# Performance work log

Hardware: AMD Instinct MI355X
Metric: run time of the kernel (lower is better)

The kernel has to match this reference:

```python
import jax, jax.numpy as jnp
import numpy as np

BETA = 0.25  # commitment loss weight (init kwarg)


def setup_inputs() -> dict:
    key = jax.random.key(0)
    k1, k2 = jax.random.split(key)
    z = jax.random.normal(k1, (16, 32, 32, 256), dtype=jnp.float32)
    embedding = jax.random.normal(k2, (8192, 256), dtype=jnp.float32)
    return {"z": z, "embedding": embedding}


def reference(z, embedding):
    # Eval-mode forward of EMAVectorQuantizer (EMA buffer update only runs in training).
    b, h, w, c = z.shape
    zf = z.reshape(-1, c)  # [N, d]
    # Squared L2 distance to every codebook entry: ||z||^2 + ||e||^2 - 2 z.e
    d = (jnp.sum(zf * zf, axis=1, keepdims=True)
         + jnp.sum(embedding * embedding, axis=1)
         - 2.0 * jnp.einsum('nd,kd->nk', zf, embedding))  # [N, n_embed]
    idx = jnp.argmin(d, axis=1)  # [N]
    z_q = embedding[idx].reshape(z.shape)  # codebook gather

    # Commitment loss (z_q is detached in the original)
    diff = BETA * jnp.mean((jax.lax.stop_gradient(z_q) - z) ** 2)

    # Straight-through estimator
    z_q = z + jax.lax.stop_gradient(z_q - z)
    z_q = jnp.transpose(z_q, (0, 3, 1, 2))  # b h w c -> b c h w

    # Perplexity as written in the source: each one-hot row contributes
    # exactly 1*log(1 + 1e-12), so the mean is a constant == exp(-log1p(1e-12)).
    perplexity = jnp.exp(-jnp.log1p(jnp.float32(1e-12)))

    return z_q, diff, idx, perplexity
```

## Files before the change

kernel.cpp:

```cpp
#include <hip/hip_runtime.h>
#include <hip/hip_bf16.h>
#include <hip/hip_fp16.h>

#define N_VEC   16384
#define K_CODES 8192
#define D_DIM   256
#define NSPLIT  8
#define KT_PER  8
#define BM      128

#define ZQ_SIZE  (16*256*32*32)
#define DIFF_OFF ZQ_SIZE
#define IDX_OFF  (ZQ_SIZE + 1)
#define PERP_OFF (ZQ_SIZE + 1 + N_VEC)

#define WS_ENORM 0
#define WS_ZH    65536
#define WS_EH    (WS_ZH + N_VEC * D_DIM * 2)
#define WS_P2    (WS_EH + K_CODES * D_DIM * 2)
#define WS_IDXI  (WS_P2 + NSPLIT * N_VEC * 16)
#define WS_LOSS  (WS_IDXI + N_VEC * 4)

typedef _Float16 f16x8 __attribute__((ext_vector_type(8)));
typedef float    f32x4 __attribute__((ext_vector_type(4)));

__device__ __forceinline__ unsigned long long skey(float s, int c) {
    unsigned u = __float_as_uint(s);
    u ^= (unsigned)((int)u >> 31) | 0x80000000u;
    return ((unsigned long long)u << 13) | (unsigned)c;
}

__device__ __forceinline__ int swz_off(int row, int dloc) {
    return row * 128 + ((((dloc >> 3) ^ (row & 7))) << 4) + ((dloc & 7) << 1);
}

__device__ __forceinline__ void gload16(const void* g, void* l) {
    __builtin_amdgcn_global_load_lds((const __attribute__((address_space(1))) unsigned int*)g,
                                     (__attribute__((address_space(3))) unsigned int*)l,
                                     16, 0, 0);
}

__global__ __launch_bounds__(256) void convert_kernel(const float* __restrict__ Z,
                                                      const float* __restrict__ E,
                                                      char* __restrict__ ws) {
    const int t  = threadIdx.x;
    const int r  = blockIdx.x * 4 + (t >> 6);
    const int d0 = (t & 63) * 4;
    const float* src;
    char* dh;
    const bool isE = (r >= N_VEC);
    if (!isE) {
        src = Z + (size_t)r * D_DIM;
        const int rowl = r & 127;
        dh = ws + WS_ZH + (size_t)(((r >> 7) * 4) + (d0 >> 6)) * 16384
           + swz_off(rowl, d0 & 63);
    } else {
        const int re = r - N_VEC;
        src = E + (size_t)re * D_DIM;
        const int col  = re & 127;
        const int k32  = d0 >> 5;
        const int dloc = d0 & 31;
        const int slot = (dloc >> 3) ^ ((col >> 1) & 3);
        dh = ws + WS_EH + (size_t)((re >> 7) * 8 + k32) * 8192
           + col * 64 + slot * 16 + (dloc & 7) * 2;
    }
    const float4 v = *reinterpret_cast<const float4*>(src + d0);
    const unsigned h0 = __half_as_ushort(__float2half(v.x));
    const unsigned h1 = __half_as_ushort(__float2half(v.y));
    const unsigned h2 = __half_as_ushort(__float2half(v.z));
    const unsigned h3 = __half_as_ushort(__float2half(v.w));
    uint2 hi;
    hi.x = h0 | (h1 << 16);  hi.y = h2 | (h3 << 16);
    *reinterpret_cast<uint2*>(dh) = hi;

    if (isE) {
        float s = v.x * v.x + v.y * v.y + v.z * v.z + v.w * v.w;
        #pragma unroll
        for (int off = 32; off; off >>= 1) s += __shfl_down(s, off);
        if ((t & 63) == 0) ((float*)(ws + WS_ENORM))[r - N_VEC] = s;
    }
}

__global__ __launch_bounds__(256, 2) void vq_mfma_kernel(const char* __restrict__ ws_ro,
                                                         ulonglong2* __restrict__ part2) {
    __shared__ short lds[40960];

    const int tid  = threadIdx.x;
    const int lane = tid & 63, wid = tid >> 6;
    const int lane15 = lane & 15, g = lane >> 4;
    const int l7  = lane15 & 7;
    const int c13 = (lane15 >> 1) & 3;
    const int wm = wid >> 1, wn = wid & 1;
    const int bx = blockIdx.x, ksp = blockIdx.y;
    const int row0 = bx * BM;
    const int kbase = ksp * (K_CODES / NSPLIT);

    const char* zh = ws_ro + WS_ZH;
    const char* eh = ws_ro + WS_EH;
    const float* enorm = (const float*)(ws_ro + WS_ENORM);

    #define STAGE_B(kt_, j_)                                                           \
    do {                                                                               \
        const char* sB = eh + (size_t)(((ksp * 8 + (kt_)) * 8) + (j_)) * 8192          \
                            + wid * 2048 + lane * 16;                                  \
        short* dB = lds + 32768 + ((j_) & 1) * 4096 + wid * 1024 + lane * 8;           \
        gload16(sB, dB);                                                               \
        gload16(sB + 1024, dB + 512);                                                  \
    } while (0)

    {
        const char* srcA = zh + (size_t)bx * 65536 + wid * 16384 + lane * 16;
        short* dA = lds + wid * 8192 + lane * 8;
        #pragma unroll
        for (int i = 0; i < 16; ++i) gload16(srcA + i * 1024, dA + i * 512);
    }
    STAGE_B(0, 0);
    float en_c[4], en_n[4];
    #pragma unroll
    for (int n = 0; n < 4; ++n) en_c[n] = enorm[kbase + wn * 64 + n * 16 + lane15];
    asm volatile("s_waitcnt vmcnt(0)" ::: "memory");
    __builtin_amdgcn_s_barrier();
    __builtin_amdgcn_sched_barrier(0);

    int rowterm[4];
    #pragma unroll
    for (int m = 0; m < 4; ++m) rowterm[m] = (wm * 64 + m * 16 + lane15) * 64;
    int colterm[4];
    #pragma unroll
    for (int n = 0; n < 4; ++n) colterm[n] = (wn * 64 + n * 16 + lane15) * 32;
    const int sa0 = (g ^ l7) * 8;
    const int sb  = (g ^ c13) * 8;

    float bestv[16];
    int   bestc[16];
    #pragma unroll
    for (int i = 0; i < 16; ++i) { bestv[i] = 3.0e38f; bestc[i] = 0; }

    #define STEP(j_)                                                                   \
    do {                                                                               \
        asm volatile("s_waitcnt vmcnt(0)" ::: "memory");                               \
        __builtin_amdgcn_s_barrier();                                                  \
        __builtin_amdgcn_sched_barrier(0);                                             \
        f16x8 af[4], bf[4];                                                            \
        const int abase = ((j_) >> 1) * 8192 + (sa0 ^ (((j_) & 1) << 5));              \
        const int bbase = 32768 + ((j_) & 1) * 4096 + sb;                              \
        _Pragma("unroll")                                                              \
        for (int m = 0; m < 4; ++m)                                                    \
            af[m] = *reinterpret_cast<const f16x8*>(lds + abase + rowterm[m]);         \
        _Pragma("unroll")                                                              \
        for (int n = 0; n < 4; ++n)                                                    \
            bf[n] = *reinterpret_cast<const f16x8*>(lds + bbase + colterm[n]);         \
        if ((j_) < 7) {                                                                \
            STAGE_B(kt, (j_) + 1);                                                     \
        } else if (kt < KT_PER - 1) {                                                  \
            STAGE_B(kt + 1, 0);                                                        \
            _Pragma("unroll")                                                          \
            for (int n = 0; n < 4; ++n)                                                \
                en_n[n] = enorm[kbase + (kt + 1) * 128 + wn * 64 + n * 16 + lane15];   \
        }                                                                              \
        __builtin_amdgcn_s_setprio(1);                                                 \
        _Pragma("unroll")                                                              \
        for (int m = 0; m < 4; ++m)                                                    \
            _Pragma("unroll")                                                          \
            for (int n = 0; n < 4; ++n)                                                \
                acc[m][n] = __builtin_amdgcn_mfma_f32_16x16x32_f16(                    \
                    af[m], bf[n], acc[m][n], 0, 0, 0);                                 \
        __builtin_amdgcn_s_setprio(0);                                                 \
    } while (0)

    for (int kt = 0; kt < KT_PER; ++kt) {
        f32x4 acc[4][4];
        #pragma unroll
        for (int m = 0; m < 4; ++m)
            #pragma unroll
            for (int n = 0; n < 4; ++n)
                #pragma unroll
                for (int q = 0; q < 4; ++q) acc[m][n][q] = 0.0f;

        STEP(0); STEP(1); STEP(2); STEP(3);
        STEP(4); STEP(5); STEP(6); STEP(7);

        #pragma unroll
        for (int m = 0; m < 4; ++m)
            #pragma unroll
            for (int n = 0; n < 4; ++n) {
                const int c = kbase + kt * 128 + wn * 64 + n * 16 + lane15;
                #pragma unroll
                for (int q = 0; q < 4; ++q) {
                    const int sl = m * 4 + q;
                    const float s = fmaf(-2.0f, acc[m][n][q], en_c[n]);
                    if (s < bestv[sl]) { bestv[sl] = s; bestc[sl] = c; }
                }
            }
        #pragma unroll
        for (int n = 0; n < 4; ++n) en_c[n] = en_n[n];
    }
    #undef STEP
    #undef STAGE_B

    unsigned long long* t2 = reinterpret_cast<unsigned long long*>(lds);
    #pragma unroll
    for (int sl = 0; sl < 16; ++sl) {
        const int m = sl >> 2, q = sl & 3;
        const unsigned long long k1 = skey(bestv[sl], bestc[sl]);
        unsigned long long m1 = k1;
        #pragma unroll
        for (int msk = 1; msk < 16; msk <<= 1) {
            const unsigned long long o = __shfl_xor(m1, msk);
            m1 = (o < m1) ? o : m1;
        }
        unsigned long long k2 = (k1 == m1) ? ~0ull : k1;
        #pragma unroll
        for (int msk = 1; msk < 16; msk <<= 1) {
            const unsigned long long o = __shfl_xor(k2, msk);
            k2 = (o < k2) ? o : k2;
        }
        if (lane15 == 0) {
            const int row64 = m * 16 + g * 4 + q;
            t2[(wid * 64 + row64) * 2 + 0] = m1;
            t2[(wid * 64 + row64) * 2 + 1] = k2;
        }
    }
    __syncthreads();
    if (tid < 128) {
        const int wm2 = tid >> 6, r64 = tid & 63;
        const unsigned long long a1 = t2[((wm2 * 2 + 0) * 64 + r64) * 2 + 0];
        const unsigned long long a2 = t2[((wm2 * 2 + 0) * 64 + r64) * 2 + 1];
        const unsigned long long b1 = t2[((wm2 * 2 + 1) * 64 + r64) * 2 + 0];
        const unsigned long long b2 = t2[((wm2 * 2 + 1) * 64 + r64) * 2 + 1];
        const unsigned long long r1 = (a1 < b1) ? a1 : b1;
        const unsigned long long hi = (a1 < b1) ? b1 : a1;
        const unsigned long long l2 = (a2 < b2) ? a2 : b2;
        const unsigned long long r2 = (hi < l2) ? hi : l2;
        ulonglong2 res;  res.x = r1;  res.y = r2;
        part2[(size_t)ksp * N_VEC + row0 + tid] = res;
    }
}

__global__ __launch_bounds__(256) void rescore_kernel(const float* __restrict__ Z,
                                                      const float* __restrict__ E,
                                                      const ulonglong2* __restrict__ part2,
                                                      int* __restrict__ idx_i,
                                                      float* __restrict__ out_idx,
                                                      float* __restrict__ lossp) {
    __shared__ double redl[4];
    const int tid = threadIdx.x, lane = tid & 63, wid = tid >> 6;
    const int r = blockIdx.x * 4 + wid;
    int c0 = 0, c1 = 0, c2 = 0, c3 = 0;
    if (lane == 0) {
        unsigned long long m0 = ~0ull, m1 = ~0ull, m2 = ~0ull, m3 = ~0ull;
        for (int s = 0; s < NSPLIT; ++s) {
            const ulonglong2 p = part2[(size_t)s * N_VEC + r];
            unsigned long long k = p.x;
            if (k < m0) { m3 = m2; m2 = m1; m1 = m0; m0 = k; }
            else if (k < m1) { m3 = m2; m2 = m1; m1 = k; }
            else if (k < m2) { m3 = m2; m2 = k; }
            else if (k < m3) { m3 = k; }
            k = p.y;
            if (k < m0) { m3 = m2; m2 = m1; m1 = m0; m0 = k; }
            else if (k < m1) { m3 = m2; m2 = m1; m1 = k; }
            else if (k < m2) { m3 = m2; m2 = k; }
            else if (k < m3) { m3 = k; }
        }
        c0 = (int)(m0 & 0x1FFFull);  c1 = (int)(m1 & 0x1FFFull);
        c2 = (int)(m2 & 0x1FFFull);  c3 = (int)(m3 & 0x1FFFull);
    }
    c0 = __shfl(c0, 0);  c1 = __shfl(c1, 0);
    c2 = __shfl(c2, 0);  c3 = __shfl(c3, 0);
    const float4 z4 = *reinterpret_cast<const float4*>(Z + (size_t)r * D_DIM + lane * 4);
    double d[4];
    const int cc[4] = {c0, c1, c2, c3};
    #pragma unroll
    for (int j = 0; j < 4; ++j) {
        const float4 e4 = *reinterpret_cast<const float4*>(E + (size_t)cc[j] * D_DIM + lane * 4);
        const double ax = (double)z4.x - (double)e4.x, ay = (double)z4.y - (double)e4.y;
        const double az = (double)z4.z - (double)e4.z, aw = (double)z4.w - (double)e4.w;
        d[j] = ax * ax + ay * ay + az * az + aw * aw;
    }
    #pragma unroll
    for (int off = 1; off < 64; off <<= 1) {
        #pragma unroll
        for (int j = 0; j < 4; ++j) d[j] += __shfl_xor(d[j], off);
    }
    if (lane == 0) {
        double bd = d[0];  int bi = c0;
        #pragma unroll
        for (int j = 1; j < 4; ++j) {
            if (d[j] < bd || (d[j] == bd && cc[j] < bi)) { bd = d[j]; bi = cc[j]; }
        }
        idx_i[r]   = bi;
        out_idx[r] = (float)bi;
        redl[wid]  = bd;
    }
    __syncthreads();
    if (tid == 0) lossp[blockIdx.x] = (float)(redl[0] + redl[1] + redl[2] + redl[3]);
}

__global__ __launch_bounds__(256) void gather_kernel(const float* __restrict__ E,
                                                     const int* __restrict__ idx_i,
                                                     float* __restrict__ out) {
    __shared__ float Ls[128 * 65];
    __shared__ int   sIdx[64];

    const int tid = threadIdx.x;
    const int gb  = blockIdx.x;
    const int n0  = gb * 64;
    const int b   = n0 >> 10;
    const int hwbase = n0 & 1023;

    if (tid < 64) sIdx[tid] = idx_i[n0 + tid];
    __syncthreads();

    for (int h = 0; h < 2; ++h) {
        if (h) __syncthreads();
        const int rowl = tid >> 2;
        const int qs   = tid & 3;
        const float* erow = E + (size_t)sIdx[rowl] * D_DIM + h * 128;
        #pragma unroll
        for (int m = 0; m < 8; ++m) {
            const int c4 = m * 4 + qs;
            const float4 v = *reinterpret_cast<const float4*>(erow + c4 * 4);
            Ls[(c4 * 4 + 0) * 65 + rowl] = v.x;
            Ls[(c4 * 4 + 1) * 65 + rowl] = v.y;
            Ls[(c4 * 4 + 2) * 65 + rowl] = v.z;
            Ls[(c4 * 4 + 3) * 65 + rowl] = v.w;
        }
        __syncthreads();
        const int wl   = tid & 63;
        const int csub = tid >> 6;
        #pragma unroll
        for (int pc = 0; pc < 32; ++pc) {
            const int c_l = pc * 4 + csub;
            const int c   = h * 128 + c_l;
            out[((size_t)(b * 256 + c)) * 1024 + hwbase + wl] = Ls[c_l * 65 + wl];
        }
    }
}

__global__ __launch_bounds__(256) void final_kernel(const float* __restrict__ lossp,
                                                    float* __restrict__ out) {
    __shared__ float red[4];
    const int tid = threadIdx.x;
    float s = 0.0f;
    for (int i = tid; i < N_VEC / 4; i += 256) s += lossp[i];
    #pragma unroll
    for (int off = 32; off; off >>= 1) s += __shfl_down(s, off);
    if ((tid & 63) == 0) red[tid >> 6] = s;
    __syncthreads();
    if (tid == 0) {
        const float total = red[0] + red[1] + red[2] + red[3];
        out[DIFF_OFF] = 0.25f * (total / (float)(N_VEC * D_DIM));
        out[PERP_OFF] = 1.0f;
    }
}

extern "C" void kernel_launch(void* const* d_in, const int* in_sizes, int n_in,
                              void* d_out, int out_size, void* d_ws, size_t ws_size,
                              hipStream_t stream) {
    const float* Z = (const float*)d_in[0];
    const float* E = (const float*)d_in[1];
    float* out = (float*)d_out;
    char*  ws  = (char*)d_ws;

    ulonglong2* part2   = (ulonglong2*)(ws + WS_P2);
    int*        idx_i   = (int*)(ws + WS_IDXI);
    float*      lossbuf = (float*)(ws + WS_LOSS);

    hipLaunchKernelGGL(convert_kernel, dim3((N_VEC + K_CODES) / 4), dim3(256), 0, stream, Z, E, ws);
    hipLaunchKernelGGL(vq_mfma_kernel, dim3(N_VEC / BM, NSPLIT), dim3(256), 0, stream,
                       (const char*)ws, part2);
    hipLaunchKernelGGL(rescore_kernel, dim3(N_VEC / 4), dim3(256), 0, stream,
                       Z, E, part2, idx_i, out + IDX_OFF, lossbuf);
    hipLaunchKernelGGL(gather_kernel, dim3(N_VEC / 64), dim3(256), 0, stream,
                       E, idx_i, out);
    hipLaunchKernelGGL(final_kernel, dim3(1), dim3(256), 0, stream, lossbuf, out);
}
```

Measured before the change: 117.5 us.

## Hold A tile in registers and stream codebook through a 4-slot LDS ring

```diff
diff --git a/kernel.cpp b/kernel.cpp
--- a/kernel.cpp
+++ b/kernel.cpp
@@ -39,6 +39,9 @@
                                      (__attribute__((address_space(3))) unsigned int*)l,
                                      16, 0, 0);
 }
+
+#define VMW__(n) asm volatile("s_waitcnt vmcnt(" #n ")" ::: "memory")
+#define VMW(n) VMW__(n)
 
 __global__ __launch_bounds__(256) void convert_kernel(const float* __restrict__ Z,
                                                       const float* __restrict__ E,
@@ -83,124 +86,127 @@
 
 __global__ __launch_bounds__(256, 2) void vq_mfma_kernel(const char* __restrict__ ws_ro,
                                                          ulonglong2* __restrict__ part2) {
-    __shared__ short lds[40960];
+    __shared__ short lds[18432];
 
     const int tid  = threadIdx.x;
     const int lane = tid & 63, wid = tid >> 6;
     const int lane15 = lane & 15, g = lane >> 4;
-    const int l7  = lane15 & 7;
     const int c13 = (lane15 >> 1) & 3;
-    const int wm = wid >> 1, wn = wid & 1;
     const int bx = blockIdx.x, ksp = blockIdx.y;
     const int row0 = bx * BM;
     const int kbase = ksp * (K_CODES / NSPLIT);
+    const int kspBase = ksp * 64;
 
     const char* zh = ws_ro + WS_ZH;
     const char* eh = ws_ro + WS_EH;
-    const float* enorm = (const float*)(ws_ro + WS_ENORM);
-
-    #define STAGE_B(kt_, j_)                                                           \
+    short* ring = lds;
+    float* enl  = (float*)(lds + 16384);
+
+    #define STAGE_SC(sc_, slot_)                                                       \
     do {                                                                               \
-        const char* sB = eh + (size_t)(((ksp * 8 + (kt_)) * 8) + (j_)) * 8192          \
-                            + wid * 2048 + lane * 16;                                  \
-        short* dB = lds + 32768 + ((j_) & 1) * 4096 + wid * 1024 + lane * 8;           \
+        const char* sB = eh + (size_t)(kspBase + (sc_)) * 8192 + wid * 2048 + lane * 16; \
+        short* dB = ring + (slot_) * 4096 + wid * 1024 + lane * 8;                     \
         gload16(sB, dB);                                                               \
         gload16(sB + 1024, dB + 512);                                                  \
     } while (0)
 
+    f16x8 areg[8][2];
     {
-        const char* srcA = zh + (size_t)bx * 65536 + wid * 16384 + lane * 16;
-        short* dA = lds + wid * 8192 + lane * 8;
-        #pragma unroll
-        for (int i = 0; i < 16; ++i) gload16(srcA + i * 1024, dA + i * 512);
-    }
-    STAGE_B(0, 0);
-    float en_c[4], en_n[4];
-    #pragma unroll
-    for (int n = 0; n < 4; ++n) en_c[n] = enorm[kbase + wn * 64 + n * 16 + lane15];
-    asm volatile("s_waitcnt vmcnt(0)" ::: "memory");
+        const char* tileA = zh + (size_t)bx * 65536;
+        #pragma unroll
+        for (int j = 0; j < 8; ++j)
+            #pragma unroll
+            for (int m = 0; m < 2; ++m) {
+                const int row  = wid * 32 + m * 16 + lane15;
+                const int slot = (((j & 1) * 4 + g)) ^ (row & 7);
+                areg[j][m] = *reinterpret_cast<const f16x8*>(
+                    tileA + (j >> 1) * 16384 + row * 128 + (slot << 4));
+            }
+    }
+    gload16((const char*)(ws_ro + WS_ENORM) + ksp * 4096 + wid * 1024 + lane * 16,
+            (char*)enl + wid * 1024 + lane * 16);
+    __builtin_amdgcn_sched_barrier(0);
+    STAGE_SC(0, 0);
+    STAGE_SC(1, 1);
+    STAGE_SC(2, 2);
+    #pragma unroll
+    for (int j = 0; j < 8; ++j)
+        #pragma unroll
+        for (int m = 0; m < 2; ++m)
+            asm volatile("" : "+v"(areg[j][m]));
+
+    int colterm[8];
+    #pragma unroll
+    for (int n = 0; n < 8; ++n) colterm[n] = (n * 16 + lane15) * 32;
+    const int sb = (g ^ c13) * 8;
+
+    float bestv[8];
+    int   bestc[8];
+    #pragma unroll
+    for (int i = 0; i < 8; ++i) { bestv[i] = 3.0e38f; bestc[i] = 0; }
+
+    VMW(6);
     __builtin_amdgcn_s_barrier();
     __builtin_amdgcn_sched_barrier(0);
 
-    int rowterm[4];
-    #pragma unroll
-    for (int m = 0; m < 4; ++m) rowterm[m] = (wm * 64 + m * 16 + lane15) * 64;
-    int colterm[4];
-    #pragma unroll
-    for (int n = 0; n < 4; ++n) colterm[n] = (wn * 64 + n * 16 + lane15) * 32;
-    const int sa0 = (g ^ l7) * 8;
-    const int sb  = (g ^ c13) * 8;
-
-    float bestv[16];
-    int   bestc[16];
-    #pragma unroll
-    for (int i = 0; i < 16; ++i) { bestv[i] = 3.0e38f; bestc[i] = 0; }
-
-    #define STEP(j_)                                                                   \
+    #define STEP(j_, c_)                                                               \
     do {                                                                               \
-        asm volatile("s_waitcnt vmcnt(0)" ::: "memory");                               \
+        VMW(c_);                                                                       \
         __builtin_amdgcn_s_barrier();                                                  \
         __builtin_amdgcn_sched_barrier(0);                                             \
-        f16x8 af[4], bf[4];                                                            \
-        const int abase = ((j_) >> 1) * 8192 + (sa0 ^ (((j_) & 1) << 5));              \
-        const int bbase = 32768 + ((j_) & 1) * 4096 + sb;                              \
+        f16x8 bf[8];                                                                   \
         _Pragma("unroll")                                                              \
-        for (int m = 0; m < 4; ++m)                                                    \
-            af[m] = *reinterpret_cast<const f16x8*>(lds + abase + rowterm[m]);         \
-        _Pragma("unroll")                                                              \
-        for (int n = 0; n < 4; ++n)                                                    \
-            bf[n] = *reinterpret_cast<const f16x8*>(lds + bbase + colterm[n]);         \
-        if ((j_) < 7) {                                                                \
-            STAGE_B(kt, (j_) + 1);                                                     \
-        } else if (kt < KT_PER - 1) {                                                  \
-            STAGE_B(kt + 1, 0);                                                        \
-            _Pragma("unroll")                                                          \
-            for (int n = 0; n < 4; ++n)                                                \
-                en_n[n] = enorm[kbase + (kt + 1) * 128 + wn * 64 + n * 16 + lane15];   \
-        }                                                                              \
+        for (int n_ = 0; n_ < 8; ++n_)                                                 \
+            bf[n_] = *reinterpret_cast<const f16x8*>(ring + ((j_) & 3) * 4096          \
+                                                     + colterm[n_] + sb);              \
+        const int sc_ = kt * 8 + (j_) + 3;                                             \
+        if (sc_ < 64) STAGE_SC(sc_, ((j_) + 3) & 3);                                   \
         __builtin_amdgcn_s_setprio(1);                                                 \
         _Pragma("unroll")                                                              \
-        for (int m = 0; m < 4; ++m)                                                    \
+        for (int m_ = 0; m_ < 2; ++m_)                                                 \
             _Pragma("unroll")                                                          \
-            for (int n = 0; n < 4; ++n)                                                \
-                acc[m][n] = __builtin_amdgcn_mfma_f32_16x16x32_f16(                    \
-                    af[m], bf[n], acc[m][n], 0, 0, 0);                                 \
+            for (int n_ = 0; n_ < 8; ++n_)                                             \
+                acc[m_][n_] = __builtin_amdgcn_mfma_f32_16x16x32_f16(                  \
+                    areg[j_][m_], bf[n_], acc[m_][n_], 0, 0, 0);                       \
         __builtin_amdgcn_s_setprio(0);                                                 \
     } while (0)
 
     for (int kt = 0; kt < KT_PER; ++kt) {
-        f32x4 acc[4][4];
-        #pragma unroll
-        for (int m = 0; m < 4; ++m)
+        float en_r[8];
+        #pragma unroll
+        for (int n = 0; n < 8; ++n) en_r[n] = enl[kt * 128 + n * 16 + lane15];
+
+        f32x4 acc[2][8];
+        #pragma unroll
+        for (int m = 0; m < 2; ++m)
             #pragma unroll
-            for (int n = 0; n < 4; ++n)
+            for (int n = 0; n < 8; ++n)
                 #pragma unroll
                 for (int q = 0; q < 4; ++q) acc[m][n][q] = 0.0f;
 
-        STEP(0); STEP(1); STEP(2); STEP(3);
-        STEP(4); STEP(5); STEP(6); STEP(7);
-
-        #pragma unroll
-        for (int m = 0; m < 4; ++m)
+        STEP(0, 4); STEP(1, 4); STEP(2, 4);
+        STEP(3, 4); STEP(4, 4); STEP(5, 4);
+        if (kt < KT_PER - 1) { STEP(6, 4); STEP(7, 4); }
+        else                 { STEP(6, 2); STEP(7, 0); }
+
+        #pragma unroll
+        for (int m = 0; m < 2; ++m)
             #pragma unroll
-            for (int n = 0; n < 4; ++n) {
-                const int c = kbase + kt * 128 + wn * 64 + n * 16 + lane15;
+            for (int n = 0; n < 8; ++n) {
+                const int c = kbase + kt * 128 + n * 16 + lane15;
                 #pragma unroll
                 for (int q = 0; q < 4; ++q) {
                     const int sl = m * 4 + q;
-                    const float s = fmaf(-2.0f, acc[m][n][q], en_c[n]);
+                    const float s = fmaf(-2.0f, acc[m][n][q], en_r[n]);
                     if (s < bestv[sl]) { bestv[sl] = s; bestc[sl] = c; }
                 }
             }
-        #pragma unroll
-        for (int n = 0; n < 4; ++n) en_c[n] = en_n[n];
     }
     #undef STEP
-    #undef STAGE_B
-
-    unsigned long long* t2 = reinterpret_cast<unsigned long long*>(lds);
-    #pragma unroll
-    for (int sl = 0; sl < 16; ++sl) {
+    #undef STAGE_SC
+
+    #pragma unroll
+    for (int sl = 0; sl < 8; ++sl) {
         const int m = sl >> 2, q = sl & 3;
         const unsigned long long k1 = skey(bestv[sl], bestc[sl]);
         unsigned long long m1 = k1;
@@ -216,24 +222,10 @@
             k2 = (o < k2) ? o : k2;
         }
         if (lane15 == 0) {
-            const int row64 = m * 16 + g * 4 + q;
-            t2[(wid * 64 + row64) * 2 + 0] = m1;
-            t2[(wid * 64 + row64) * 2 + 1] = k2;
-        }
-    }
-    __syncthreads();
-    if (tid < 128) {
-        const int wm2 = tid >> 6, r64 = tid & 63;
-        const unsigned long long a1 = t2[((wm2 * 2 + 0) * 64 + r64) * 2 + 0];
-        const unsigned long long a2 = t2[((wm2 * 2 + 0) * 64 + r64) * 2 + 1];
-        const unsigned long long b1 = t2[((wm2 * 2 + 1) * 64 + r64) * 2 + 0];
-        const unsigned long long b2 = t2[((wm2 * 2 + 1) * 64 + r64) * 2 + 1];
-        const unsigned long long r1 = (a1 < b1) ? a1 : b1;
-        const unsigned long long hi = (a1 < b1) ? b1 : a1;
-        const unsigned long long l2 = (a2 < b2) ? a2 : b2;
-        const unsigned long long r2 = (hi < l2) ? hi : l2;
-        ulonglong2 res;  res.x = r1;  res.y = r2;
-        part2[(size_t)ksp * N_VEC + row0 + tid] = res;
+            const int row = row0 + wid * 32 + m * 16 + g * 4 + q;
+            ulonglong2 res;  res.x = m1;  res.y = k2;
+            part2[(size_t)ksp * N_VEC + row] = res;
+        }
     }
 }
 
```

Result: slower. 152.8 us (+30.1%).

## Widen VQ MFMA block to 512 threads with 256-code tiles and triple-buffered ring

Applied to the files above, without the earlier changes.

```diff
diff --git a/kernel.cpp b/kernel.cpp
--- a/kernel.cpp
+++ b/kernel.cpp
@@ -6,7 +6,6 @@
 #define K_CODES 8192
 #define D_DIM   256
 #define NSPLIT  8
-#define KT_PER  8
 #define BM      128
 
 #define ZQ_SIZE  (16*256*32*32)
@@ -39,6 +38,9 @@
                                      (__attribute__((address_space(3))) unsigned int*)l,
                                      16, 0, 0);
 }
+
+#define VMW__(n) asm volatile("s_waitcnt vmcnt(" #n ")" ::: "memory")
+#define VMW(n) VMW__(n)
 
 __global__ __launch_bounds__(256) void convert_kernel(const float* __restrict__ Z,
                                                       const float* __restrict__ E,
@@ -81,94 +83,97 @@
     }
 }
 
-__global__ __launch_bounds__(256, 2) void vq_mfma_kernel(const char* __restrict__ ws_ro,
+__global__ __launch_bounds__(512, 2) void vq_mfma_kernel(const char* __restrict__ ws_ro,
                                                          ulonglong2* __restrict__ part2) {
-    __shared__ short lds[40960];
+    __shared__ short lds[59392];
 
     const int tid  = threadIdx.x;
     const int lane = tid & 63, wid = tid >> 6;
     const int lane15 = lane & 15, g = lane >> 4;
     const int l7  = lane15 & 7;
-    const int c13 = (lane15 >> 1) & 3;
-    const int wm = wid >> 1, wn = wid & 1;
+    const int wm = wid >> 2, wn = wid & 3;
     const int bx = blockIdx.x, ksp = blockIdx.y;
     const int row0 = bx * BM;
     const int kbase = ksp * (K_CODES / NSPLIT);
 
     const char* zh = ws_ro + WS_ZH;
     const char* eh = ws_ro + WS_EH;
-    const float* enorm = (const float*)(ws_ro + WS_ENORM);
-
-    #define STAGE_B(kt_, j_)                                                           \
+    short* ring = lds + 32768;
+    float* enl  = (float*)(lds + 57344);
+
+    #define STAGE_SC(sc_, slot_)                                                       \
     do {                                                                               \
-        const char* sB = eh + (size_t)(((ksp * 8 + (kt_)) * 8) + (j_)) * 8192          \
-                            + wid * 2048 + lane * 16;                                  \
-        short* dB = lds + 32768 + ((j_) & 1) * 4096 + wid * 1024 + lane * 8;           \
-        gload16(sB, dB);                                                               \
-        gload16(sB + 1024, dB + 512);                                                  \
+        if ((sc_) < 32) {                                                              \
+            const int cg_ = (sc_) >> 3, j_ = (sc_) & 7;                                \
+            const char* s0 = eh + (size_t)(((ksp * 8 + cg_ * 2) * 8) + j_) * 8192      \
+                                + wid * 1024 + lane * 16;                              \
+            short* d_ = ring + (slot_) * 8192 + wid * 512 + lane * 8;                  \
+            gload16(s0, d_);                                                           \
+            gload16(s0 + 65536, d_ + 4096);                                            \
+        }                                                                              \
     } while (0)
 
     {
-        const char* srcA = zh + (size_t)bx * 65536 + wid * 16384 + lane * 16;
-        short* dA = lds + wid * 8192 + lane * 8;
-        #pragma unroll
-        for (int i = 0; i < 16; ++i) gload16(srcA + i * 1024, dA + i * 512);
-    }
-    STAGE_B(0, 0);
-    float en_c[4], en_n[4];
-    #pragma unroll
-    for (int n = 0; n < 4; ++n) en_c[n] = enorm[kbase + wn * 64 + n * 16 + lane15];
-    asm volatile("s_waitcnt vmcnt(0)" ::: "memory");
+        const char* srcA = zh + (size_t)bx * 65536 + wid * 8192 + lane * 16;
+        short* dA = lds + wid * 4096 + lane * 8;
+        #pragma unroll
+        for (int i = 0; i < 8; ++i) gload16(srcA + i * 1024, dA + i * 512);
+    }
+    gload16((const char*)(ws_ro + WS_ENORM) + ksp * 4096 + (wid & 3) * 1024 + lane * 16,
+            (char*)enl + (wid & 3) * 1024 + lane * 16);
+    __builtin_amdgcn_sched_barrier(0);
+    STAGE_SC(0, 0);
+    STAGE_SC(1, 1);
+
+    int rowterm[4];
+    #pragma unroll
+    for (int m = 0; m < 4; ++m) rowterm[m] = (wm * 64 + m * 16 + lane15) * 64;
+    const int sa0 = (g ^ l7) * 8;
+    int boff[4];
+    #pragma unroll
+    for (int n = 0; n < 4; ++n) {
+        const int cl   = wn * 64 + n * 16 + lane15;
+        const int c127 = cl & 127;
+        boff[n] = (cl >> 7) * 4096 + c127 * 32 + ((g ^ ((c127 >> 1) & 3)) << 3);
+    }
+
+    float bestv[16];
+    int   bestc[16];
+    #pragma unroll
+    for (int i = 0; i < 16; ++i) { bestv[i] = 3.0e38f; bestc[i] = 0; }
+
+    VMW(2);
     __builtin_amdgcn_s_barrier();
     __builtin_amdgcn_sched_barrier(0);
 
-    int rowterm[4];
-    #pragma unroll
-    for (int m = 0; m < 4; ++m) rowterm[m] = (wm * 64 + m * 16 + lane15) * 64;
-    int colterm[4];
-    #pragma unroll
-    for (int n = 0; n < 4; ++n) colterm[n] = (wn * 64 + n * 16 + lane15) * 32;
-    const int sa0 = (g ^ l7) * 8;
-    const int sb  = (g ^ c13) * 8;
-
-    float bestv[16];
-    int   bestc[16];
-    #pragma unroll
-    for (int i = 0; i < 16; ++i) { bestv[i] = 3.0e38f; bestc[i] = 0; }
-
-    #define STEP(j_)                                                                   \
+    #define STEP(cg_, j_)                                                              \
     do {                                                                               \
-        asm volatile("s_waitcnt vmcnt(0)" ::: "memory");                               \
+        const int s_ = (cg_) * 8 + (j_);                                               \
+        if (s_ == 31) { VMW(0); } else { VMW(2); }                                     \
         __builtin_amdgcn_s_barrier();                                                  \
         __builtin_amdgcn_sched_barrier(0);                                             \
         f16x8 af[4], bf[4];                                                            \
         const int abase = ((j_) >> 1) * 8192 + (sa0 ^ (((j_) & 1) << 5));              \
-        const int bbase = 32768 + ((j_) & 1) * 4096 + sb;                              \
+        const int bbase = (s_ % 3) * 8192;                                             \
         _Pragma("unroll")                                                              \
-        for (int m = 0; m < 4; ++m)                                                    \
-            af[m] = *reinterpret_cast<const f16x8*>(lds + abase + rowterm[m]);         \
+        for (int m_ = 0; m_ < 4; ++m_)                                                 \
+            af[m_] = *reinterpret_cast<const f16x8*>(lds + abase + rowterm[m_]);       \
         _Pragma("unroll")                                                              \
-        for (int n = 0; n < 4; ++n)                                                    \
-            bf[n] = *reinterpret_cast<const f16x8*>(lds + bbase + colterm[n]);         \
-        if ((j_) < 7) {                                                                \
-            STAGE_B(kt, (j_) + 1);                                                     \
-        } else if (kt < KT_PER - 1) {                                                  \
-            STAGE_B(kt + 1, 0);                                                        \
-            _Pragma("unroll")                                                          \
-            for (int n = 0; n < 4; ++n)                                                \
-                en_n[n] = enorm[kbase + (kt + 1) * 128 + wn * 64 + n * 16 + lane15];   \
-        }                                                                              \
+        for (int n_ = 0; n_ < 4; ++n_)                                                 \
+            bf[n_] = *reinterpret_cast<const f16x8*>(ring + bbase + boff[n_]);         \
+        STAGE_SC(s_ + 2, (s_ + 2) % 3);                                                \
         __builtin_amdgcn_s_setprio(1);                                                 \
         _Pragma("unroll")                                                              \
-        for (int m = 0; m < 4; ++m)                                                    \
+        for (int m_ = 0; m_ < 4; ++m_)                                                 \
             _Pragma("unroll")                                                          \
-            for (int n = 0; n < 4; ++n)                                                \
-                acc[m][n] = __builtin_amdgcn_mfma_f32_16x16x32_f16(                    \
-                    af[m], bf[n], acc[m][n], 0, 0, 0);                                 \
+            for (int n_ = 0; n_ < 4; ++n_)                                             \
+                acc[m_][n_] = __builtin_amdgcn_mfma_f32_16x16x32_f16(                  \
+                    af[m_], bf[n_], acc[m_][n_], 0, 0, 0);                             \
         __builtin_amdgcn_s_setprio(0);                                                 \
     } while (0)
 
-    for (int kt = 0; kt < KT_PER; ++kt) {
+    #pragma unroll
+    for (int cg = 0; cg < 4; ++cg) {
         f32x4 acc[4][4];
         #pragma unroll
         for (int m = 0; m < 4; ++m)
@@ -177,27 +182,28 @@
                 #pragma unroll
                 for (int q = 0; q < 4; ++q) acc[m][n][q] = 0.0f;
 
-        STEP(0); STEP(1); STEP(2); STEP(3);
-        STEP(4); STEP(5); STEP(6); STEP(7);
+        STEP(cg, 0); STEP(cg, 1); STEP(cg, 2); STEP(cg, 3);
+        STEP(cg, 4); STEP(cg, 5); STEP(cg, 6); STEP(cg, 7);
 
         #pragma unroll
         for (int m = 0; m < 4; ++m)
             #pragma unroll
             for (int n = 0; n < 4; ++n) {
-                const int c = kbase + kt * 128 + wn * 64 + n * 16 + lane15;
+                const int cl = cg * 256 + wn * 64 + n * 16 + lane15;
+                const int c  = kbase + cl;
+                const float en = enl[cl];
                 #pragma unroll
                 for (int q = 0; q < 4; ++q) {
                     const int sl = m * 4 + q;
-                    const float s = fmaf(-2.0f, acc[m][n][q], en_c[n]);
+                    const float s = fmaf(-2.0f, acc[m][n][q], en);
                     if (s < bestv[sl]) { bestv[sl] = s; bestc[sl] = c; }
                 }
             }
-        #pragma unroll
-        for (int n = 0; n < 4; ++n) en_c[n] = en_n[n];
     }
     #undef STEP
-    #undef STAGE_B
-
+    #undef STAGE_SC
+
+    __syncthreads();
     unsigned long long* t2 = reinterpret_cast<unsigned long long*>(lds);
     #pragma unroll
     for (int sl = 0; sl < 16; ++sl) {
@@ -223,17 +229,19 @@
     }
     __syncthreads();
     if (tid < 128) {
-        const int wm2 = tid >> 6, r64 = tid & 63;
-        const unsigned long long a1 = t2[((wm2 * 2 + 0) * 64 + r64) * 2 + 0];
-        const unsigned long long a2 = t2[((wm2 * 2 + 0) * 64 + r64) * 2 + 1];
-        const unsigned long long b1 = t2[((wm2 * 2 + 1) * 64 + r64) * 2 + 0];
-        const unsigned long long b2 = t2[((wm2 * 2 + 1) * 64 + r64) * 2 + 1];
-        const unsigned long long r1 = (a1 < b1) ? a1 : b1;
-        const unsigned long long hi = (a1 < b1) ? b1 : a1;
-        const unsigned long long l2 = (a2 < b2) ? a2 : b2;
-        const unsigned long long r2 = (hi < l2) ? hi : l2;
-        ulonglong2 res;  res.x = r1;  res.y = r2;
-        part2[(size_t)ksp * N_VEC + row0 + tid] = res;
+        const int wmg = tid >> 6, r64 = tid & 63;
+        unsigned long long m0 = ~0ull, m1 = ~0ull;
+        #pragma unroll
+        for (int w = 0; w < 4; ++w) {
+            #pragma unroll
+            for (int k = 0; k < 2; ++k) {
+                const unsigned long long key = t2[(((wmg * 4 + w) * 64) + r64) * 2 + k];
+                if (key < m0) { m1 = m0; m0 = key; }
+                else if (key < m1) { m1 = key; }
+            }
+        }
+        ulonglong2 res;  res.x = m0;  res.y = m1;
+        part2[(size_t)ksp * N_VEC + row0 + wmg * 64 + r64] = res;
     }
 }
 
@@ -367,7 +375,7 @@
     float*      lossbuf = (float*)(ws + WS_LOSS);
 
     hipLaunchKernelGGL(convert_kernel, dim3((N_VEC + K_CODES) / 4), dim3(256), 0, stream, Z, E, ws);
-    hipLaunchKernelGGL(vq_mfma_kernel, dim3(N_VEC / BM, NSPLIT), dim3(256), 0, stream,
+    hipLaunchKernelGGL(vq_mfma_kernel, dim3(N_VEC / BM, NSPLIT), dim3(512), 0, stream,
                        (const char*)ws, part2);
     hipLaunchKernelGGL(rescore_kernel, dim3(N_VEC / 4), dim3(256), 0, stream,
                        Z, E, part2, idx_i, out + IDX_OFF, lossbuf);
```

Result: slower. 147.3 us (+25.4%).

## Switch to 16x16x16 MFMA with a 4-slot codebook ring and partial waits

Applied to the files above, without the earlier changes.

```diff
diff --git a/kernel.cpp b/kernel.cpp
--- a/kernel.cpp
+++ b/kernel.cpp
@@ -21,7 +21,7 @@
 #define WS_IDXI  (WS_P2 + NSPLIT * N_VEC * 16)
 #define WS_LOSS  (WS_IDXI + N_VEC * 4)
 
-typedef _Float16 f16x8 __attribute__((ext_vector_type(8)));
+typedef _Float16 f16x4 __attribute__((ext_vector_type(4)));
 typedef float    f32x4 __attribute__((ext_vector_type(4)));
 
 __device__ __forceinline__ unsigned long long skey(float s, int c) {
@@ -39,6 +39,9 @@
                                      (__attribute__((address_space(3))) unsigned int*)l,
                                      16, 0, 0);
 }
+
+#define VMW__(n) asm volatile("s_waitcnt vmcnt(" #n ")" ::: "memory")
+#define VMW(n) VMW__(n)
 
 __global__ __launch_bounds__(256) void convert_kernel(const float* __restrict__ Z,
                                                       const float* __restrict__ E,
@@ -57,12 +60,10 @@
     } else {
         const int re = r - N_VEC;
         src = E + (size_t)re * D_DIM;
-        const int col  = re & 127;
-        const int k32  = d0 >> 5;
-        const int dloc = d0 & 31;
-        const int slot = (dloc >> 3) ^ ((col >> 1) & 3);
-        dh = ws + WS_EH + (size_t)((re >> 7) * 8 + k32) * 8192
-           + col * 64 + slot * 16 + (dloc & 7) * 2;
+        const int col = re & 127;
+        const int q   = (d0 >> 2) & 3;
+        dh = ws + WS_EH + (size_t)((re >> 7) * 16 + (d0 >> 4)) * 4096
+           + col * 32 + ((q ^ ((col >> 2) & 3)) << 3);
     }
     const float4 v = *reinterpret_cast<const float4*>(src + d0);
     const unsigned h0 = __half_as_ushort(__float2half(v.x));
@@ -88,8 +89,7 @@
     const int tid  = threadIdx.x;
     const int lane = tid & 63, wid = tid >> 6;
     const int lane15 = lane & 15, g = lane >> 4;
-    const int l7  = lane15 & 7;
-    const int c13 = (lane15 >> 1) & 3;
+    const int g1 = g >> 1;
     const int wm = wid >> 1, wn = wid & 1;
     const int bx = blockIdx.x, ksp = blockIdx.y;
     const int row0 = bx * BM;
@@ -98,14 +98,13 @@
     const char* zh = ws_ro + WS_ZH;
     const char* eh = ws_ro + WS_EH;
     const float* enorm = (const float*)(ws_ro + WS_ENORM);
-
-    #define STAGE_B(kt_, j_)                                                           \
+    short* ring = lds + 32768;
+
+    #define STAGE_C(kt_, pp_)                                                          \
     do {                                                                               \
-        const char* sB = eh + (size_t)(((ksp * 8 + (kt_)) * 8) + (j_)) * 8192          \
-                            + wid * 2048 + lane * 16;                                  \
-        short* dB = lds + 32768 + ((j_) & 1) * 4096 + wid * 1024 + lane * 8;           \
-        gload16(sB, dB);                                                               \
-        gload16(sB + 1024, dB + 512);                                                  \
+        const char* sC = eh + (size_t)(((ksp * 8 + (kt_)) * 16) + (pp_)) * 4096        \
+                            + tid * 16;                                                \
+        gload16(sC, ring + ((pp_) & 3) * 2048 + tid * 8);                              \
     } while (0)
 
     {
@@ -114,57 +113,56 @@
         #pragma unroll
         for (int i = 0; i < 16; ++i) gload16(srcA + i * 1024, dA + i * 512);
     }
-    STAGE_B(0, 0);
-    float en_c[4], en_n[4];
-    #pragma unroll
-    for (int n = 0; n < 4; ++n) en_c[n] = enorm[kbase + wn * 64 + n * 16 + lane15];
-    asm volatile("s_waitcnt vmcnt(0)" ::: "memory");
+    STAGE_C(0, 0);
+    STAGE_C(0, 1);
+    VMW(1);
     __builtin_amdgcn_s_barrier();
     __builtin_amdgcn_sched_barrier(0);
 
-    int rowterm[4];
-    #pragma unroll
-    for (int m = 0; m < 4; ++m) rowterm[m] = (wm * 64 + m * 16 + lane15) * 64;
-    int colterm[4];
-    #pragma unroll
-    for (int n = 0; n < 4; ++n) colterm[n] = (wn * 64 + n * 16 + lane15) * 32;
-    const int sa0 = (g ^ l7) * 8;
-    const int sb  = (g ^ c13) * 8;
+    int rowbase[4], r7[4];
+    #pragma unroll
+    for (int m = 0; m < 4; ++m) {
+        const int row = wm * 64 + m * 16 + lane15;
+        rowbase[m] = row * 64 + 4 * (g & 1);
+        r7[m]      = row & 7;
+    }
+    int boffn[4];
+    #pragma unroll
+    for (int n = 0; n < 4; ++n) {
+        const int col = wn * 64 + n * 16 + lane15;
+        boffn[n] = col * 16 + ((g ^ ((col >> 2) & 3)) << 2);
+    }
 
     float bestv[16];
     int   bestc[16];
     #pragma unroll
     for (int i = 0; i < 16; ++i) { bestv[i] = 3.0e38f; bestc[i] = 0; }
 
-    #define STEP(j_)                                                                   \
+    #define STEP(p_)                                                                   \
     do {                                                                               \
-        asm volatile("s_waitcnt vmcnt(0)" ::: "memory");                               \
+        if ((p_) == 15 && kt == KT_PER - 1) { VMW(0); } else { VMW(1); }               \
         __builtin_amdgcn_s_barrier();                                                  \
         __builtin_amdgcn_sched_barrier(0);                                             \
-        f16x8 af[4], bf[4];                                                            \
-        const int abase = ((j_) >> 1) * 8192 + (sa0 ^ (((j_) & 1) << 5));              \
-        const int bbase = 32768 + ((j_) & 1) * 4096 + sb;                              \
+        f16x4 af[4], bf[4];                                                            \
+        const int abase = ((p_) >> 2) * 8192;                                          \
+        const int op    = ((p_) & 3) * 2;                                              \
         _Pragma("unroll")                                                              \
-        for (int m = 0; m < 4; ++m)                                                    \
-            af[m] = *reinterpret_cast<const f16x8*>(lds + abase + rowterm[m]);         \
+        for (int m_ = 0; m_ < 4; ++m_)                                                 \
+            af[m_] = *reinterpret_cast<const f16x4*>(                                  \
+                lds + abase + rowbase[m_] + (((op + g1) ^ r7[m_]) << 3));              \
         _Pragma("unroll")                                                              \
-        for (int n = 0; n < 4; ++n)                                                    \
-            bf[n] = *reinterpret_cast<const f16x8*>(lds + bbase + colterm[n]);         \
-        if ((j_) < 7) {                                                                \
-            STAGE_B(kt, (j_) + 1);                                                     \
-        } else if (kt < KT_PER - 1) {                                                  \
-            STAGE_B(kt + 1, 0);                                                        \
-            _Pragma("unroll")                                                          \
-            for (int n = 0; n < 4; ++n)                                                \
-                en_n[n] = enorm[kbase + (kt + 1) * 128 + wn * 64 + n * 16 + lane15];   \
-        }                                                                              \
+        for (int n_ = 0; n_ < 4; ++n_)                                                 \
+            bf[n_] = *reinterpret_cast<const f16x4*>(                                  \
+                ring + ((p_) & 3) * 2048 + boffn[n_]);                                 \
+        if ((p_) < 14)                STAGE_C(kt, (p_) + 2);                           \
+        else if (kt < KT_PER - 1)     STAGE_C(kt + 1, (p_) - 14);                      \
         __builtin_amdgcn_s_setprio(1);                                                 \
         _Pragma("unroll")                                                              \
-        for (int m = 0; m < 4; ++m)                                                    \
+        for (int m_ = 0; m_ < 4; ++m_)                                                 \
             _Pragma("unroll")                                                          \
-            for (int n = 0; n < 4; ++n)                                                \
-                acc[m][n] = __builtin_amdgcn_mfma_f32_16x16x32_f16(                    \
-                    af[m], bf[n], acc[m][n], 0, 0, 0);                                 \
+            for (int n_ = 0; n_ < 4; ++n_)                                             \
+                acc[m_][n_] = __builtin_amdgcn_mfma_f32_16x16x16f16(                   \
+                    af[m_], bf[n_], acc[m_][n_], 0, 0, 0);                             \
         __builtin_amdgcn_s_setprio(0);                                                 \
     } while (0)
 
@@ -177,26 +175,27 @@
                 #pragma unroll
                 for (int q = 0; q < 4; ++q) acc[m][n][q] = 0.0f;
 
-        STEP(0); STEP(1); STEP(2); STEP(3);
-        STEP(4); STEP(5); STEP(6); STEP(7);
-
-        #pragma unroll
-        for (int m = 0; m < 4; ++m)
+        STEP(0);  STEP(1);  STEP(2);  STEP(3);
+        STEP(4);  STEP(5);  STEP(6);  STEP(7);
+        STEP(8);  STEP(9);  STEP(10); STEP(11);
+        STEP(12); STEP(13); STEP(14); STEP(15);
+
+        #pragma unroll
+        for (int n = 0; n < 4; ++n) {
+            const int c  = kbase + kt * 128 + wn * 64 + n * 16 + lane15;
+            const float en = enorm[c];
             #pragma unroll
-            for (int n = 0; n < 4; ++n) {
-                const int c = kbase + kt * 128 + wn * 64 + n * 16 + lane15;
+            for (int m = 0; m < 4; ++m)
                 #pragma unroll
                 for (int q = 0; q < 4; ++q) {
                     const int sl = m * 4 + q;
-                    const float s = fmaf(-2.0f, acc[m][n][q], en_c[n]);
+                    const float s = fmaf(-2.0f, acc[m][n][q], en);
                     if (s < bestv[sl]) { bestv[sl] = s; bestc[sl] = c; }
                 }
-            }
-        #pragma unroll
-        for (int n = 0; n < 4; ++n) en_c[n] = en_n[n];
+        }
     }
     #undef STEP
-    #undef STAGE_B
+    #undef STAGE_C
 
     unsigned long long* t2 = reinterpret_cast<unsigned long long*>(lds);
     #pragma unroll
```

Measured after the change: 148.0 us. 1.26x slower.
